# Kernel tuning notes

Measured on AMD Instinct MI355X. Metric: run time of the kernel, lower is better.

The kernel has to match this reference:

```python
import jax, jax.numpy as jnp
import numpy as np
import math

B, S, D, N, H = 4, 2048, 1024, 512, 8
HD = D // H  # head_dim = 128
LN_EPS = 1e-5


def setup_inputs() -> dict:
    key = jax.random.key(0)
    ks = jax.random.split(key, 12)
    return {
        "query": jax.random.normal(ks[0], (B, S, D), jnp.float32),
        "memory_weights": jax.random.uniform(ks[1], (B, S, N), jnp.float32),
        "update_input": jax.random.normal(ks[2], (B, S, D), jnp.float32),
        "memory_keys": jax.random.normal(ks[3], (N, D), jnp.float32),
        "memory_values": jax.random.normal(ks[4], (N, D), jnp.float32),
        "memory_decay": jnp.float32(0.95),
        "gate_w": jax.random.normal(ks[5], (2 * D, D), jnp.float32) / math.sqrt(2 * D),
        "gate_b": jnp.zeros((D,), jnp.float32),
        "out_w": jax.random.normal(ks[6], (D, D), jnp.float32) / math.sqrt(D),
        "out_b": jnp.zeros((D,), jnp.float32),
        "ln_gamma": jnp.ones((D,), jnp.float32),
        "ln_beta": jnp.zeros((D,), jnp.float32),
    }


def reference(query, memory_weights, update_input, memory_keys, memory_values,
              memory_decay, gate_w, gate_b, out_w, out_b, ln_gamma, ln_beta):
    # Multi-head attention read: einsum 'bshd,nhd->bsn' sums over h and d,
    # so it equals a full [D]-dot product; only the scale uses head_dim.
    scores = jnp.einsum("bsd,nd->bsn", query, memory_keys) / math.sqrt(HD)
    scores = scores * memory_weights  # multiplicative mask before softmax
    probs = jax.nn.softmax(scores, axis=-1)
    memory_read = jnp.einsum("bsn,nd->bsd", probs, memory_values)
    memory_read = memory_read * memory_decay

    # Gated update path (update_input provided)
    gate_in = jnp.concatenate([memory_read, update_input], axis=-1)  # [B,S,2D]
    gate = jax.nn.sigmoid(gate_in @ gate_w + gate_b)  # [B,S,D]
    # NOTE: the no_grad EMA update of memory_values is a side effect that does
    # not influence this forward output; omitted from the pure reference.
    memory_read = memory_read * (1.0 + jnp.mean(gate, axis=-1, keepdims=True))

    out = memory_read @ out_w + out_b  # output projection (dropout = eval identity)
    mu = jnp.mean(out, axis=-1, keepdims=True)
    var = jnp.var(out, axis=-1, keepdims=True)
    out = (out - mu) * jax.lax.rsqrt(var + LN_EPS) * ln_gamma + ln_beta
    return out
```

## Files before the change

### kernel.cpp

```cpp
#include <hip/hip_runtime.h>
#include <hip/hip_bf16.h>

typedef __attribute__((ext_vector_type(8))) short bf16x8;
typedef __attribute__((ext_vector_type(4))) float f32x4;
typedef __attribute__((ext_vector_type(4))) int i32x4;
typedef __attribute__((ext_vector_type(2))) int i32x2;
typedef __attribute__((ext_vector_type(4))) unsigned short u16x4;

static __device__ __forceinline__ void gload_lds16(const void* g, void* l) {
  __builtin_amdgcn_global_load_lds((const __attribute__((address_space(1))) void*)g,
                                   (__attribute__((address_space(3))) void*)l,
                                   16, 0, 0);
}

static __device__ __forceinline__ unsigned short f2bf(float x) {
  unsigned int u = __float_as_uint(x);
  u += 0x7fffu + ((u >> 16) & 1u);
  return (unsigned short)(u >> 16);
}
static __device__ __forceinline__ float bf2f(unsigned short u) {
  return __uint_as_float((unsigned int)u << 16);
}

__global__ __launch_bounds__(256)
void prep(const float* __restrict__ ob, int* __restrict__ flag,
          float* __restrict__ zeros,
          const float* __restrict__ mk, const float* __restrict__ mv,
          unsigned short* __restrict__ kb, unsigned short* __restrict__ mvb,
          const float* __restrict__ ow, unsigned short* __restrict__ owt,
          const float* __restrict__ q, unsigned short* __restrict__ qb)
{
  __shared__ float t[32][33];
  const int b = blockIdx.x;
  const int tid = threadIdx.x;
  if (b == 0) {
    f32x4 v = *(const f32x4*)(ob + tid * 4);
    float mx = fmaxf(fmaxf(fabsf(v[0]), fabsf(v[1])), fmaxf(fabsf(v[2]), fabsf(v[3])));
#pragma unroll
    for (int off = 32; off >= 1; off >>= 1) mx = fmaxf(mx, __shfl_xor(mx, off, 64));
    __shared__ float sm[4];
    const int wid = tid >> 6, lane = tid & 63;
    if (lane == 0) sm[wid] = mx;
    __syncthreads();
    if (tid == 0) {
      float m = fmaxf(fmaxf(sm[0], sm[1]), fmaxf(sm[2], sm[3]));
      *flag = (m != 0.0f) ? 1 : 0;
    }
  } else if (b < 17) {
    f32x4 z = {};
    *(f32x4*)(zeros + (b - 1) * 1024 + tid * 4) = z;
  } else if (b < 529) {
    int idx = (b - 17) * 256 + tid;
    const float* in; unsigned short* out; int rel;
    if (idx < 65536) { in = mk; out = kb;  rel = idx; }
    else             { in = mv; out = mvb; rel = idx - 65536; }
    size_t f = (size_t)rel * 8;
    f32x4 a = *(const f32x4*)(in + f);
    f32x4 c = *(const f32x4*)(in + f + 4);
    union { unsigned short u[8]; i32x4 vec; } pk;
#pragma unroll
    for (int i = 0; i < 4; ++i) { pk.u[i] = f2bf(a[i]); pk.u[4 + i] = f2bf(c[i]); }
    *(i32x4*)(out + f) = pk.vec;
  } else if (b < 1553) {
    int id = b - 529;
    const int bx = id & 31, by = id >> 5;
    const int tx = tid & 31, ty = tid >> 5;
    const int c0 = bx * 32, r0 = by * 32;
#pragma unroll
    for (int i = 0; i < 4; ++i)
      t[ty + i * 8][tx] = ow[(size_t)(r0 + ty + i * 8) * 1024 + c0 + tx];
    __syncthreads();
#pragma unroll
    for (int i = 0; i < 4; ++i)
      owt[(size_t)(c0 + ty + i * 8) * 1024 + r0 + tx] = f2bf(t[tx][ty + i * 8]);
  } else {
    int idx = (b - 1553) * 256 + tid;
    size_t f = (size_t)idx * 8;
    f32x4 a = *(const f32x4*)(q + f);
    f32x4 c = *(const f32x4*)(q + f + 4);
    union { unsigned short u[8]; i32x4 vec; } pk;
#pragma unroll
    for (int i = 0; i < 4; ++i) { pk.u[i] = f2bf(a[i]); pk.u[4 + i] = f2bf(c[i]); }
    *(i32x4*)(qb + f) = pk.vec;
  }
}

__global__ __launch_bounds__(256)
void prep_gated(const float* __restrict__ upd, unsigned short* __restrict__ cat,
                const float* __restrict__ gw, unsigned short* __restrict__ gwt,
                const float* __restrict__ mv, unsigned short* __restrict__ vt,
                const int* __restrict__ flag)
{
  if (*flag == 0) return;
  __shared__ float t[32][33];
  const int b = blockIdx.x;
  const int tid = threadIdx.x;
  if (b < 4096) {
    int idx = b * 256 + tid;
    size_t f = (size_t)idx * 8;
    int row = (int)(f >> 10);
    int col = (int)(f & 1023);
    f32x4 a = *(const f32x4*)(upd + f);
    f32x4 c = *(const f32x4*)(upd + f + 4);
    union { unsigned short u[8]; i32x4 vec; } pk;
#pragma unroll
    for (int i = 0; i < 4; ++i) { pk.u[i] = f2bf(a[i]); pk.u[4 + i] = f2bf(c[i]); }
    *(i32x4*)(cat + (size_t)row * 2048 + 1024 + col) = pk.vec;
  } else {
    const float* in; unsigned short* out; int R, id;
    if (b < 6144) { in = gw; out = gwt; R = 2048; id = b - 4096; }
    else          { in = mv; out = vt;  R = 512;  id = b - 6144; }
    const int bx = id & 31, by = id >> 5;
    const int tx = tid & 31, ty = tid >> 5;
    const int c0 = bx * 32, r0 = by * 32;
#pragma unroll
    for (int i = 0; i < 4; ++i)
      t[ty + i * 8][tx] = in[(size_t)(r0 + ty + i * 8) * 1024 + c0 + tx];
    __syncthreads();
#pragma unroll
    for (int i = 0; i < 4; ++i)
      out[(size_t)(c0 + ty + i * 8) * R + r0 + tx] = f2bf(t[tx][ty + i * 8]);
  }
}

template <int EPI, int BN>
__global__ __launch_bounds__(256)
void gemm_bt(const unsigned short* __restrict__ A, int lda,
             const unsigned short* __restrict__ Bt, int ldb,
             int Kd, int Nd,
             unsigned short* __restrict__ Cb, int ldcb,
             const float* __restrict__ bias,
             float* __restrict__ rowsum,
             const float* __restrict__ fscale,
             const int* __restrict__ flag)
{
  if (flag != nullptr && *flag == 0) return;
  constexpr int NB = BN / 32;
  __shared__ unsigned short As[128 * 64];
  __shared__ unsigned short Bs[BN * 64];
  const int tid  = threadIdx.x;
  const int wid  = tid >> 6;
  const int lane = tid & 63;

  const int nwg  = gridDim.x * gridDim.y;
  const int flat = blockIdx.y * gridDim.x + blockIdx.x;
  const int swz  = (flat & 7) * (nwg >> 3) + (flat >> 3);
  const int bx   = swz % gridDim.x;
  const int by   = swz / gridDim.x;

  const int brow = by * 128;
  const int bcol = bx * BN;
  const int wr = wid >> 1, wc = wid & 1;
  const int l15 = lane & 15, l4 = lane >> 4;

  f32x4 acc[4][NB] = {};
  const int foff = wid * 512 + lane * 8;

  for (int k0 = 0; k0 < Kd; k0 += 64) {
#pragma unroll
    for (int c = 0; c < 4; ++c) {
      int f = c * 2048 + foff;
      int r = f >> 6, kc = f & 63;
      gload_lds16(A + (size_t)(brow + r) * lda + k0 + kc, As + c * 2048 + wid * 512);
    }
#pragma unroll
    for (int c = 0; c < NB; ++c) {
      int f = c * 2048 + foff;
      int r = f >> 6, kc = f & 63;
      gload_lds16(Bt + (size_t)(bcol + r) * ldb + k0 + kc, Bs + c * 2048 + wid * 512);
    }
    __syncthreads();
#pragma unroll
    for (int kk = 0; kk < 2; ++kk) {
      const int ko = kk * 32 + l4 * 8;
      bf16x8 af[4], bfv[NB];
#pragma unroll
      for (int m = 0; m < 4; ++m)
        af[m] = *(const bf16x8*)(As + (wr * 64 + m * 16 + l15) * 64 + ko);
#pragma unroll
      for (int n = 0; n < NB; ++n)
        bfv[n] = *(const bf16x8*)(Bs + (wc * (BN / 2) + n * 16 + l15) * 64 + ko);
#pragma unroll
      for (int m = 0; m < 4; ++m)
#pragma unroll
        for (int n = 0; n < NB; ++n)
          acc[m][n] = __builtin_amdgcn_mfma_f32_16x16x32_bf16(af[m], bfv[n], acc[m][n], 0, 0, 0);
    }
    __syncthreads();
  }

  if constexpr (EPI == 2) {
#pragma unroll
    for (int m = 0; m < 4; ++m) {
#pragma unroll
      for (int j = 0; j < 4; ++j) {
        float part = 0.0f;
#pragma unroll
        for (int n = 0; n < NB; ++n) {
          int col = bcol + wc * (BN / 2) + n * 16 + l15;
          float x = acc[m][n][j] + bias[col];
          part += 1.0f / (1.0f + __expf(-x));
        }
#pragma unroll
        for (int off = 1; off < 16; off <<= 1)
          part += __shfl_xor(part, off, 64);
        if (l15 == 0) {
          int row = brow + wr * 64 + m * 16 + l4 * 4 + j;
          atomicAdd(&rowsum[row], part);
        }
      }
    }
  } else if constexpr (EPI == 5) {
#pragma unroll
    for (int m = 0; m < 4; ++m) {
#pragma unroll
      for (int j = 0; j < 4; ++j) {
        int row = brow + wr * 64 + m * 16 + l4 * 4 + j;
        const float* mwrow = bias + (size_t)row * Nd;
        float part = 0.0f;
#pragma unroll
        for (int n = 0; n < NB; ++n) {
          int col = bcol + wc * (BN / 2) + n * 16 + l15;
          float p = __expf(acc[m][n][j] * 0.08838834764831845f * mwrow[col]);
          part += p;
          Cb[(size_t)row * ldcb + col] = f2bf(p);
        }
#pragma unroll
        for (int off = 1; off < 16; off <<= 1)
          part += __shfl_xor(part, off, 64);
        if (l15 == 0) atomicAdd(&rowsum[row], part);
      }
    }
  } else {
    float fs = 1.0f;
    if constexpr (EPI == 1) fs = *fscale;
#pragma unroll
    for (int m = 0; m < 4; ++m) {
      int row0 = brow + wr * 64 + m * 16 + l4 * 4;
#pragma unroll
      for (int j = 0; j < 4; ++j) {
        int row = row0 + j;
        const float rscl = fs / rowsum[row];
#pragma unroll
        for (int n = 0; n < NB; ++n) {
          int col = bcol + wc * (BN / 2) + n * 16 + l15;
          Cb[(size_t)row * ldcb + col] = f2bf(acc[m][n][j] * rscl);
        }
      }
    }
  }
}

__global__ __launch_bounds__(256)
void w2_partial(const unsigned short* __restrict__ owt,
                const unsigned short* __restrict__ mvb,
                float* __restrict__ w2p)
{
  __shared__ unsigned short As[128 * 64];
  __shared__ unsigned short Bs[128 * 64];
  const int tid  = threadIdx.x;
  const int wid  = tid >> 6;
  const int lane = tid & 63;
  const int brow = blockIdx.y * 128;
  const int bcol = blockIdx.x * 128;
  const int kbeg = blockIdx.z * 128;
  const int wr = wid >> 1, wc = wid & 1;
  const int l15 = lane & 15, l4 = lane >> 4;

  f32x4 acc[4][4] = {};
  const int foff = wid * 512 + lane * 8;

  for (int k0 = kbeg; k0 < kbeg + 128; k0 += 64) {
#pragma unroll
    for (int c = 0; c < 4; ++c) {
      int f = c * 2048 + foff;
      int r = f >> 6, kc = f & 63;
      gload_lds16(owt + (size_t)(brow + r) * 1024 + k0 + kc, As + c * 2048 + wid * 512);
    }
#pragma unroll
    for (int c = 0; c < 4; ++c) {
      int f = c * 2048 + foff;
      int r = f >> 6, kc = f & 63;
      gload_lds16(mvb + (size_t)(bcol + r) * 1024 + k0 + kc, Bs + c * 2048 + wid * 512);
    }
    __syncthreads();
#pragma unroll
    for (int kk = 0; kk < 2; ++kk) {
      const int ko = kk * 32 + l4 * 8;
      bf16x8 af[4], bfv[4];
#pragma unroll
      for (int m = 0; m < 4; ++m)
        af[m] = *(const bf16x8*)(As + (wr * 64 + m * 16 + l15) * 64 + ko);
#pragma unroll
      for (int n = 0; n < 4; ++n)
        bfv[n] = *(const bf16x8*)(Bs + (wc * 64 + n * 16 + l15) * 64 + ko);
#pragma unroll
      for (int m = 0; m < 4; ++m)
#pragma unroll
        for (int n = 0; n < 4; ++n)
          acc[m][n] = __builtin_amdgcn_mfma_f32_16x16x32_bf16(af[m], bfv[n], acc[m][n], 0, 0, 0);
    }
    __syncthreads();
  }

  float* dst = w2p + (size_t)blockIdx.z * 524288;
#pragma unroll
  for (int m = 0; m < 4; ++m) {
    int row0 = brow + wr * 64 + m * 16 + l4 * 4;
#pragma unroll
    for (int j = 0; j < 4; ++j) {
      int row = row0 + j;
#pragma unroll
      for (int n = 0; n < 4; ++n) {
        int col = bcol + wc * 64 + n * 16 + l15;
        dst[(size_t)row * 512 + col] = acc[m][n][j];
      }
    }
  }
}

__global__ __launch_bounds__(256)
void w2_reduce(const float* __restrict__ w2p, unsigned short* __restrict__ w2t,
               const float* __restrict__ dec)
{
  const int i = (blockIdx.x * 256 + threadIdx.x) * 4;
  const float d = *dec;
  f32x4 s = {};
#pragma unroll
  for (int sl = 0; sl < 8; ++sl) {
    f32x4 p = *(const f32x4*)(w2p + (size_t)sl * 524288 + i);
    s[0] += p[0]; s[1] += p[1]; s[2] += p[2]; s[3] += p[3];
  }
  union { unsigned short u[4]; i32x2 v; } pk;
#pragma unroll
  for (int j = 0; j < 4; ++j) pk.u[j] = f2bf(s[j] * d);
  *(i32x2*)(w2t + i) = pk.v;
}

__global__ __launch_bounds__(256)
void ln_rows(const unsigned short* __restrict__ X, const float* __restrict__ gsum,
             const float* __restrict__ ob,
             const float* __restrict__ gamma, const float* __restrict__ beta,
             float* __restrict__ Y)
{
  const int row = blockIdx.x;
  const int tid = threadIdx.x;
  const size_t base = (size_t)row * 1024 + tid * 4;
  const float scl = 1.0f + gsum[row] * (1.0f / 1024.0f);
  u16x4 xr = *(const u16x4*)(X + base);
  f32x4 bo = *(const f32x4*)(ob + tid * 4);
  float x[4];
#pragma unroll
  for (int i = 0; i < 4; ++i) x[i] = bf2f(xr[i]) * scl + bo[i];
  float s = x[0] + x[1] + x[2] + x[3];
  float q = x[0] * x[0] + x[1] * x[1] + x[2] * x[2] + x[3] * x[3];
#pragma unroll
  for (int off = 32; off >= 1; off >>= 1) {
    s += __shfl_xor(s, off, 64);
    q += __shfl_xor(q, off, 64);
  }
  __shared__ float ss[4], qq[4];
  const int wid = tid >> 6, lane = tid & 63;
  if (lane == 0) { ss[wid] = s; qq[wid] = q; }
  __syncthreads();
  s = ss[0] + ss[1] + ss[2] + ss[3];
  q = qq[0] + qq[1] + qq[2] + qq[3];
  const float mu = s * (1.0f / 1024.0f);
  const float var = q * (1.0f / 1024.0f) - mu * mu;
  const float r = rsqrtf(var + 1e-5f);
  f32x4 g = *(const f32x4*)(gamma + tid * 4);
  f32x4 b = *(const f32x4*)(beta + tid * 4);
  f32x4 y;
#pragma unroll
  for (int i = 0; i < 4; ++i) y[i] = (x[i] - mu) * r * g[i] + b[i];
  *(f32x4*)(Y + base) = y;
}

extern "C" void kernel_launch(void* const* d_in, const int* in_sizes, int n_in,
                              void* d_out, int out_size, void* d_ws, size_t ws_size,
                              hipStream_t stream)
{
  (void)in_sizes; (void)n_in; (void)out_size; (void)ws_size;
  const float* q   = (const float*)d_in[0];
  const float* mw  = (const float*)d_in[1];
  const float* upd = (const float*)d_in[2];
  const float* mk  = (const float*)d_in[3];
  const float* mv  = (const float*)d_in[4];
  const float* dec = (const float*)d_in[5];
  const float* gw  = (const float*)d_in[6];
  const float* gb  = (const float*)d_in[7];
  const float* ow  = (const float*)d_in[8];
  const float* ob  = (const float*)d_in[9];
  const float* lg  = (const float*)d_in[10];
  const float* lb  = (const float*)d_in[11];
  float* outp = (float*)d_out;
  char* ws = (char*)d_ws;

  unsigned short* qb     = (unsigned short*)(ws + 0);
  unsigned short* probs  = (unsigned short*)(ws + 16777216);
  unsigned short* outpre = (unsigned short*)(ws + 25165824);
  unsigned short* kb     = (unsigned short*)(ws + 41943040);
  unsigned short* mvb    = (unsigned short*)(ws + 42991616);
  unsigned short* owt    = (unsigned short*)(ws + 44040192);
  unsigned short* w2t    = (unsigned short*)(ws + 46137344);
  float*          w2p    = (float*)(ws + 47185920);
  unsigned short* vt     = (unsigned short*)(ws + 63963136);
  unsigned short* gwt    = (unsigned short*)(ws + 65011712);
  unsigned short* cat    = (unsigned short*)(ws + 69206016);
  float*          gsum   = (float*)(ws + 102760448);
  float*          rowsum = (float*)(ws + 102793216);
  int*            flag   = (int*)(ws + 102825984);

  prep<<<5649, 256, 0, stream>>>(ob, flag, gsum, mk, mv, kb, mvb, ow, owt, q, qb);
  prep_gated<<<6656, 256, 0, stream>>>(upd, cat, gw, gwt, mv, vt, flag);

  gemm_bt<5, 64><<<dim3(8, 64), 256, 0, stream>>>(qb, 1024, kb, 1024, 1024, 512,
                                                  probs, 512, mw, rowsum, nullptr, nullptr);
  w2_partial<<<dim3(4, 8, 8), 256, 0, stream>>>(owt, mvb, w2p);
  w2_reduce<<<512, 256, 0, stream>>>(w2p, w2t, dec);
  gemm_bt<1, 128><<<dim3(8, 64), 256, 0, stream>>>(probs, 512, vt, 512, 512, 1024,
                                                   cat, 2048, nullptr, rowsum, dec, flag);
  gemm_bt<2, 128><<<dim3(8, 64), 256, 0, stream>>>(cat, 2048, gwt, 2048, 2048, 1024,
                                                   nullptr, 0, gb, gsum, nullptr, flag);
  gemm_bt<6, 128><<<dim3(8, 64), 256, 0, stream>>>(probs, 512, w2t, 512, 512, 1024,
                                                   outpre, 1024, nullptr, rowsum, nullptr, nullptr);
  ln_rows<<<8192, 256, 0, stream>>>(outpre, gsum, ob, lg, lb, outp);
}
```

Measured before the change: 88.08 us.

## Merge independent GEMM stages into shared launches to cut kernel count

Independent stages are packed into shared grids. The two prep kernels become one launch, where the gated-path blocks recompute the out_b nonzero check locally. The scores GEMM shares a launch with a 4-way split-K W2 partial GEMM, the W2 reduction shares one with the memory-read GEMM, and the output projection shares one with the gate GEMM. This cuts launches from nine to five and lets independent work fill the machine together, at the cost of fewer split-K slices and heterogeneous blocks within a grid.

```diff
diff --git a/kernel.cpp b/kernel.cpp
--- a/kernel.cpp
+++ b/kernel.cpp
@@ -20,6 +20,55 @@
 }
 static __device__ __forceinline__ float bf2f(unsigned short u) {
   return __uint_as_float((unsigned int)u << 16);
+}
+
+template <int BN>
+static __device__ __forceinline__ void gemm_core(
+    const unsigned short* __restrict__ A, int lda,
+    const unsigned short* __restrict__ Bt, int ldb,
+    int kbeg, int kend, int brow, int bcol,
+    unsigned short* As, unsigned short* Bs,
+    f32x4 (&acc)[4][BN / 32])
+{
+  constexpr int NB = BN / 32;
+  const int tid = threadIdx.x;
+  const int wid = tid >> 6, lane = tid & 63;
+  const int wr = wid >> 1, wc = wid & 1;
+  const int l15 = lane & 15, l4 = lane >> 4;
+  const int foff = wid * 512 + lane * 8;
+
+  for (int k0 = kbeg; k0 < kend; k0 += 64) {
+#pragma unroll
+    for (int c = 0; c < 4; ++c) {
+      int f = c * 2048 + foff;
+      gload_lds16(A + (size_t)(brow + (f >> 6)) * lda + k0 + (f & 63),
+                  As + c * 2048 + wid * 512);
+    }
+#pragma unroll
+    for (int c = 0; c < NB; ++c) {
+      int f = c * 2048 + foff;
+      gload_lds16(Bt + (size_t)(bcol + (f >> 6)) * ldb + k0 + (f & 63),
+                  Bs + c * 2048 + wid * 512);
+    }
+    __syncthreads();
+#pragma unroll
+    for (int kk = 0; kk < 2; ++kk) {
+      const int ko = kk * 32 + l4 * 8;
+      bf16x8 af[4], bfv[NB];
+#pragma unroll
+      for (int m = 0; m < 4; ++m)
+        af[m] = *(const bf16x8*)(As + (wr * 64 + m * 16 + l15) * 64 + ko);
+#pragma unroll
+      for (int n = 0; n < NB; ++n)
+        bfv[n] = *(const bf16x8*)(Bs + (wc * (BN / 2) + n * 16 + l15) * 64 + ko);
+#pragma unroll
+      for (int m = 0; m < 4; ++m)
+#pragma unroll
+        for (int n = 0; n < NB; ++n)
+          acc[m][n] = __builtin_amdgcn_mfma_f32_16x16x32_bf16(af[m], bfv[n], acc[m][n], 0, 0, 0);
+    }
+    __syncthreads();
+  }
 }
 
 __global__ __launch_bounds__(256)
@@ -28,7 +77,10 @@
           const float* __restrict__ mk, const float* __restrict__ mv,
           unsigned short* __restrict__ kb, unsigned short* __restrict__ mvb,
           const float* __restrict__ ow, unsigned short* __restrict__ owt,
-          const float* __restrict__ q, unsigned short* __restrict__ qb)
+          const float* __restrict__ q, unsigned short* __restrict__ qb,
+          const float* __restrict__ upd, unsigned short* __restrict__ cat,
+          const float* __restrict__ gw, unsigned short* __restrict__ gwt,
+          unsigned short* __restrict__ vt)
 {
   __shared__ float t[32][33];
   const int b = blockIdx.x;
@@ -73,7 +125,7 @@
 #pragma unroll
     for (int i = 0; i < 4; ++i)
       owt[(size_t)(c0 + ty + i * 8) * 1024 + r0 + tx] = f2bf(t[tx][ty + i * 8]);
-  } else {
+  } else if (b < 5649) {
     int idx = (b - 1553) * 256 + tid;
     size_t f = (size_t)idx * 8;
     f32x4 a = *(const f32x4*)(q + f);
@@ -82,123 +134,224 @@
 #pragma unroll
     for (int i = 0; i < 4; ++i) { pk.u[i] = f2bf(a[i]); pk.u[4 + i] = f2bf(c[i]); }
     *(i32x4*)(qb + f) = pk.vec;
+  } else {
+    f32x4 v = *(const f32x4*)(ob + tid * 4);
+    float mx = fmaxf(fmaxf(fabsf(v[0]), fabsf(v[1])), fmaxf(fabsf(v[2]), fabsf(v[3])));
+#pragma unroll
+    for (int off = 32; off >= 1; off >>= 1) mx = fmaxf(mx, __shfl_xor(mx, off, 64));
+    __shared__ float sm2[4];
+    const int wid = tid >> 6, lane = tid & 63;
+    if (lane == 0) sm2[wid] = mx;
+    __syncthreads();
+    float m = fmaxf(fmaxf(sm2[0], sm2[1]), fmaxf(sm2[2], sm2[3]));
+    if (m == 0.0f) return;
+    __syncthreads();
+    int g = b - 5649;
+    if (g < 4096) {
+      int idx = g * 256 + tid;
+      size_t f = (size_t)idx * 8;
+      int row = (int)(f >> 10);
+      int col = (int)(f & 1023);
+      f32x4 a = *(const f32x4*)(upd + f);
+      f32x4 c = *(const f32x4*)(upd + f + 4);
+      union { unsigned short u[8]; i32x4 vec; } pk;
+#pragma unroll
+      for (int i = 0; i < 4; ++i) { pk.u[i] = f2bf(a[i]); pk.u[4 + i] = f2bf(c[i]); }
+      *(i32x4*)(cat + (size_t)row * 2048 + 1024 + col) = pk.vec;
+    } else {
+      const float* in; unsigned short* out; int R, id;
+      if (g < 6144) { in = gw; out = gwt; R = 2048; id = g - 4096; }
+      else          { in = mv; out = vt;  R = 512;  id = g - 6144; }
+      const int bx = id & 31, by = id >> 5;
+      const int tx = tid & 31, ty = tid >> 5;
+      const int c0 = bx * 32, r0 = by * 32;
+#pragma unroll
+      for (int i = 0; i < 4; ++i)
+        t[ty + i * 8][tx] = in[(size_t)(r0 + ty + i * 8) * 1024 + c0 + tx];
+      __syncthreads();
+#pragma unroll
+      for (int i = 0; i < 4; ++i)
+        out[(size_t)(c0 + ty + i * 8) * R + r0 + tx] = f2bf(t[tx][ty + i * 8]);
+    }
   }
 }
 
 __global__ __launch_bounds__(256)
-void prep_gated(const float* __restrict__ upd, unsigned short* __restrict__ cat,
-                const float* __restrict__ gw, unsigned short* __restrict__ gwt,
-                const float* __restrict__ mv, unsigned short* __restrict__ vt,
-                const int* __restrict__ flag)
-{
-  if (*flag == 0) return;
-  __shared__ float t[32][33];
+void k_scores_w2(const unsigned short* __restrict__ qb,
+                 const unsigned short* __restrict__ kb,
+                 const float* __restrict__ mw,
+                 unsigned short* __restrict__ probs,
+                 float* __restrict__ rowsum,
+                 const unsigned short* __restrict__ owt,
+                 const unsigned short* __restrict__ mvb,
+                 float* __restrict__ w2p)
+{
+  __shared__ unsigned short As[128 * 64];
+  __shared__ unsigned short Bs[128 * 64];
   const int b = blockIdx.x;
   const int tid = threadIdx.x;
-  if (b < 4096) {
-    int idx = b * 256 + tid;
-    size_t f = (size_t)idx * 8;
-    int row = (int)(f >> 10);
-    int col = (int)(f & 1023);
-    f32x4 a = *(const f32x4*)(upd + f);
-    f32x4 c = *(const f32x4*)(upd + f + 4);
-    union { unsigned short u[8]; i32x4 vec; } pk;
-#pragma unroll
-    for (int i = 0; i < 4; ++i) { pk.u[i] = f2bf(a[i]); pk.u[4 + i] = f2bf(c[i]); }
-    *(i32x4*)(cat + (size_t)row * 2048 + 1024 + col) = pk.vec;
-  } else {
-    const float* in; unsigned short* out; int R, id;
-    if (b < 6144) { in = gw; out = gwt; R = 2048; id = b - 4096; }
-    else          { in = mv; out = vt;  R = 512;  id = b - 6144; }
-    const int bx = id & 31, by = id >> 5;
-    const int tx = tid & 31, ty = tid >> 5;
-    const int c0 = bx * 32, r0 = by * 32;
-#pragma unroll
-    for (int i = 0; i < 4; ++i)
-      t[ty + i * 8][tx] = in[(size_t)(r0 + ty + i * 8) * 1024 + c0 + tx];
-    __syncthreads();
-#pragma unroll
-    for (int i = 0; i < 4; ++i)
-      out[(size_t)(c0 + ty + i * 8) * R + r0 + tx] = f2bf(t[tx][ty + i * 8]);
-  }
-}
-
-template <int EPI, int BN>
-__global__ __launch_bounds__(256)
-void gemm_bt(const unsigned short* __restrict__ A, int lda,
-             const unsigned short* __restrict__ Bt, int ldb,
-             int Kd, int Nd,
-             unsigned short* __restrict__ Cb, int ldcb,
-             const float* __restrict__ bias,
-             float* __restrict__ rowsum,
-             const float* __restrict__ fscale,
-             const int* __restrict__ flag)
-{
-  if (flag != nullptr && *flag == 0) return;
-  constexpr int NB = BN / 32;
-  __shared__ unsigned short As[128 * 64];
-  __shared__ unsigned short Bs[BN * 64];
-  const int tid  = threadIdx.x;
-  const int wid  = tid >> 6;
-  const int lane = tid & 63;
-
-  const int nwg  = gridDim.x * gridDim.y;
-  const int flat = blockIdx.y * gridDim.x + blockIdx.x;
-  const int swz  = (flat & 7) * (nwg >> 3) + (flat >> 3);
-  const int bx   = swz % gridDim.x;
-  const int by   = swz / gridDim.x;
-
-  const int brow = by * 128;
-  const int bcol = bx * BN;
+  const int wid = tid >> 6, lane = tid & 63;
   const int wr = wid >> 1, wc = wid & 1;
   const int l15 = lane & 15, l4 = lane >> 4;
 
-  f32x4 acc[4][NB] = {};
-  const int foff = wid * 512 + lane * 8;
-
-  for (int k0 = 0; k0 < Kd; k0 += 64) {
-#pragma unroll
-    for (int c = 0; c < 4; ++c) {
-      int f = c * 2048 + foff;
-      int r = f >> 6, kc = f & 63;
-      gload_lds16(A + (size_t)(brow + r) * lda + k0 + kc, As + c * 2048 + wid * 512);
-    }
-#pragma unroll
-    for (int c = 0; c < NB; ++c) {
-      int f = c * 2048 + foff;
-      int r = f >> 6, kc = f & 63;
-      gload_lds16(Bt + (size_t)(bcol + r) * ldb + k0 + kc, Bs + c * 2048 + wid * 512);
-    }
-    __syncthreads();
-#pragma unroll
-    for (int kk = 0; kk < 2; ++kk) {
-      const int ko = kk * 32 + l4 * 8;
-      bf16x8 af[4], bfv[NB];
-#pragma unroll
-      for (int m = 0; m < 4; ++m)
-        af[m] = *(const bf16x8*)(As + (wr * 64 + m * 16 + l15) * 64 + ko);
-#pragma unroll
-      for (int n = 0; n < NB; ++n)
-        bfv[n] = *(const bf16x8*)(Bs + (wc * (BN / 2) + n * 16 + l15) * 64 + ko);
-#pragma unroll
-      for (int m = 0; m < 4; ++m)
-#pragma unroll
-        for (int n = 0; n < NB; ++n)
-          acc[m][n] = __builtin_amdgcn_mfma_f32_16x16x32_bf16(af[m], bfv[n], acc[m][n], 0, 0, 0);
-    }
-    __syncthreads();
-  }
-
-  if constexpr (EPI == 2) {
+  if (b < 128) {
+    const int brow = ((b >> 2) & 7) * 128;
+    const int bcol = (b & 3) * 128;
+    const int kbeg = (b >> 5) * 256;
+    f32x4 acc[4][4] = {};
+    gemm_core<128>(owt, 1024, mvb, 1024, kbeg, kbeg + 256, brow, bcol, As, Bs, acc);
+    float* dst = w2p + (size_t)(b >> 5) * 524288;
+#pragma unroll
+    for (int m = 0; m < 4; ++m) {
+      int row0 = brow + wr * 64 + m * 16 + l4 * 4;
+#pragma unroll
+      for (int j = 0; j < 4; ++j) {
+#pragma unroll
+        for (int n = 0; n < 4; ++n)
+          dst[(size_t)(row0 + j) * 512 + bcol + wc * 64 + n * 16 + l15] = acc[m][n][j];
+      }
+    }
+  } else {
+    const int f = b - 128;
+    const int swz = (f & 7) * 64 + (f >> 3);
+    const int bx = swz & 7, by = swz >> 3;
+    const int brow = by * 128, bcol = bx * 64;
+    f32x4 acc[4][2] = {};
+    gemm_core<64>(qb, 1024, kb, 1024, 0, 1024, brow, bcol, As, Bs, acc);
+#pragma unroll
+    for (int m = 0; m < 4; ++m) {
+#pragma unroll
+      for (int j = 0; j < 4; ++j) {
+        int row = brow + wr * 64 + m * 16 + l4 * 4 + j;
+        const float* mwrow = mw + (size_t)row * 512;
+        float part = 0.0f;
+#pragma unroll
+        for (int n = 0; n < 2; ++n) {
+          int col = bcol + wc * 32 + n * 16 + l15;
+          float p = __expf(acc[m][n][j] * 0.08838834764831845f * mwrow[col]);
+          part += p;
+          probs[(size_t)row * 512 + col] = f2bf(p);
+        }
+#pragma unroll
+        for (int off = 1; off < 16; off <<= 1)
+          part += __shfl_xor(part, off, 64);
+        if (l15 == 0) atomicAdd(&rowsum[row], part);
+      }
+    }
+  }
+}
+
+__global__ __launch_bounds__(256)
+void k_w2red_read(const float* __restrict__ w2p, unsigned short* __restrict__ w2t,
+                  const float* __restrict__ dec,
+                  const unsigned short* __restrict__ probs,
+                  const unsigned short* __restrict__ vt,
+                  unsigned short* __restrict__ cat,
+                  const float* __restrict__ rowsum,
+                  const int* __restrict__ flag)
+{
+  __shared__ unsigned short As[128 * 64];
+  __shared__ unsigned short Bs[128 * 64];
+  const int b = blockIdx.x;
+  const int tid = threadIdx.x;
+  if (b < 512) {
+    const int i = (b * 256 + tid) * 4;
+    const float d = *dec;
+    f32x4 s = {};
+#pragma unroll
+    for (int sl = 0; sl < 4; ++sl) {
+      f32x4 p = *(const f32x4*)(w2p + (size_t)sl * 524288 + i);
+      s[0] += p[0]; s[1] += p[1]; s[2] += p[2]; s[3] += p[3];
+    }
+    union { unsigned short u[4]; i32x2 v; } pk;
+#pragma unroll
+    for (int j = 0; j < 4; ++j) pk.u[j] = f2bf(s[j] * d);
+    *(i32x2*)(w2t + i) = pk.v;
+  } else {
+    if (*flag == 0) return;
+    const int f = b - 512;
+    const int swz = (f & 7) * 64 + (f >> 3);
+    const int bx = swz & 7, by = swz >> 3;
+    const int brow = by * 128, bcol = bx * 128;
+    const int wid = tid >> 6, lane = tid & 63;
+    const int wr = wid >> 1, wc = wid & 1;
+    const int l15 = lane & 15, l4 = lane >> 4;
+    f32x4 acc[4][4] = {};
+    gemm_core<128>(probs, 512, vt, 512, 0, 512, brow, bcol, As, Bs, acc);
+    const float d = *dec;
+#pragma unroll
+    for (int m = 0; m < 4; ++m) {
+      int row0 = brow + wr * 64 + m * 16 + l4 * 4;
+#pragma unroll
+      for (int j = 0; j < 4; ++j) {
+        int row = row0 + j;
+        const float rscl = d / rowsum[row];
+#pragma unroll
+        for (int n = 0; n < 4; ++n) {
+          int col = bcol + wc * 64 + n * 16 + l15;
+          cat[(size_t)row * 2048 + col] = f2bf(acc[m][n][j] * rscl);
+        }
+      }
+    }
+  }
+}
+
+__global__ __launch_bounds__(256)
+void k_out_gate(const unsigned short* __restrict__ probs,
+                const unsigned short* __restrict__ w2t,
+                const float* __restrict__ rowsum,
+                unsigned short* __restrict__ outpre,
+                const unsigned short* __restrict__ cat,
+                const unsigned short* __restrict__ gwt,
+                const float* __restrict__ gb,
+                float* __restrict__ gsum,
+                const int* __restrict__ flag)
+{
+  __shared__ unsigned short As[128 * 64];
+  __shared__ unsigned short Bs[128 * 64];
+  const int b = blockIdx.x;
+  const int tid = threadIdx.x;
+  const int wid = tid >> 6, lane = tid & 63;
+  const int wr = wid >> 1, wc = wid & 1;
+  const int l15 = lane & 15, l4 = lane >> 4;
+
+  if (b < 512) {
+    const int swz = (b & 7) * 64 + (b >> 3);
+    const int bx = swz & 7, by = swz >> 3;
+    const int brow = by * 128, bcol = bx * 128;
+    f32x4 acc[4][4] = {};
+    gemm_core<128>(probs, 512, w2t, 512, 0, 512, brow, bcol, As, Bs, acc);
+#pragma unroll
+    for (int m = 0; m < 4; ++m) {
+      int row0 = brow + wr * 64 + m * 16 + l4 * 4;
+#pragma unroll
+      for (int j = 0; j < 4; ++j) {
+        int row = row0 + j;
+        const float rscl = 1.0f / rowsum[row];
+#pragma unroll
+        for (int n = 0; n < 4; ++n) {
+          int col = bcol + wc * 64 + n * 16 + l15;
+          outpre[(size_t)row * 1024 + col] = f2bf(acc[m][n][j] * rscl);
+        }
+      }
+    }
+  } else {
+    if (*flag == 0) return;
+    const int f = b - 512;
+    const int swz = (f & 7) * 64 + (f >> 3);
+    const int bx = swz & 7, by = swz >> 3;
+    const int brow = by * 128, bcol = bx * 128;
+    f32x4 acc[4][4] = {};
+    gemm_core<128>(cat, 2048, gwt, 2048, 0, 2048, brow, bcol, As, Bs, acc);
 #pragma unroll
     for (int m = 0; m < 4; ++m) {
 #pragma unroll
       for (int j = 0; j < 4; ++j) {
         float part = 0.0f;
 #pragma unroll
-        for (int n = 0; n < NB; ++n) {
-          int col = bcol + wc * (BN / 2) + n * 16 + l15;
-          float x = acc[m][n][j] + bias[col];
+        for (int n = 0; n < 4; ++n) {
+          int col = bcol + wc * 64 + n * 16 + l15;
+          float x = acc[m][n][j] + gb[col];
           part += 1.0f / (1.0f + __expf(-x));
         }
 #pragma unroll
@@ -206,135 +359,11 @@
           part += __shfl_xor(part, off, 64);
         if (l15 == 0) {
           int row = brow + wr * 64 + m * 16 + l4 * 4 + j;
-          atomicAdd(&rowsum[row], part);
+          atomicAdd(&gsum[row], part);
         }
       }
     }
-  } else if constexpr (EPI == 5) {
-#pragma unroll
-    for (int m = 0; m < 4; ++m) {
-#pragma unroll
-      for (int j = 0; j < 4; ++j) {
-        int row = brow + wr * 64 + m * 16 + l4 * 4 + j;
-        const float* mwrow = bias + (size_t)row * Nd;
-        float part = 0.0f;
-#pragma unroll
-        for (int n = 0; n < NB; ++n) {
-          int col = bcol + wc * (BN / 2) + n * 16 + l15;
-          float p = __expf(acc[m][n][j] * 0.08838834764831845f * mwrow[col]);
-          part += p;
-          Cb[(size_t)row * ldcb + col] = f2bf(p);
-        }
-#pragma unroll
-        for (int off = 1; off < 16; off <<= 1)
-          part += __shfl_xor(part, off, 64);
-        if (l15 == 0) atomicAdd(&rowsum[row], part);
-      }
-    }
-  } else {
-    float fs = 1.0f;
-    if constexpr (EPI == 1) fs = *fscale;
-#pragma unroll
-    for (int m = 0; m < 4; ++m) {
-      int row0 = brow + wr * 64 + m * 16 + l4 * 4;
-#pragma unroll
-      for (int j = 0; j < 4; ++j) {
-        int row = row0 + j;
-        const float rscl = fs / rowsum[row];
-#pragma unroll
-        for (int n = 0; n < NB; ++n) {
-          int col = bcol + wc * (BN / 2) + n * 16 + l15;
-          Cb[(size_t)row * ldcb + col] = f2bf(acc[m][n][j] * rscl);
-        }
-      }
-    }
-  }
-}
-
-__global__ __launch_bounds__(256)
-void w2_partial(const unsigned short* __restrict__ owt,
-                const unsigned short* __restrict__ mvb,
-                float* __restrict__ w2p)
-{
-  __shared__ unsigned short As[128 * 64];
-  __shared__ unsigned short Bs[128 * 64];
-  const int tid  = threadIdx.x;
-  const int wid  = tid >> 6;
-  const int lane = tid & 63;
-  const int brow = blockIdx.y * 128;
-  const int bcol = blockIdx.x * 128;
-  const int kbeg = blockIdx.z * 128;
-  const int wr = wid >> 1, wc = wid & 1;
-  const int l15 = lane & 15, l4 = lane >> 4;
-
-  f32x4 acc[4][4] = {};
-  const int foff = wid * 512 + lane * 8;
-
-  for (int k0 = kbeg; k0 < kbeg + 128; k0 += 64) {
-#pragma unroll
-    for (int c = 0; c < 4; ++c) {
-      int f = c * 2048 + foff;
-      int r = f >> 6, kc = f & 63;
-      gload_lds16(owt + (size_t)(brow + r) * 1024 + k0 + kc, As + c * 2048 + wid * 512);
-    }
-#pragma unroll
-    for (int c = 0; c < 4; ++c) {
-      int f = c * 2048 + foff;
-      int r = f >> 6, kc = f & 63;
-      gload_lds16(mvb + (size_t)(bcol + r) * 1024 + k0 + kc, Bs + c * 2048 + wid * 512);
-    }
-    __syncthreads();
-#pragma unroll
-    for (int kk = 0; kk < 2; ++kk) {
-      const int ko = kk * 32 + l4 * 8;
-      bf16x8 af[4], bfv[4];
-#pragma unroll
-      for (int m = 0; m < 4; ++m)
-        af[m] = *(const bf16x8*)(As + (wr * 64 + m * 16 + l15) * 64 + ko);
-#pragma unroll
-      for (int n = 0; n < 4; ++n)
-        bfv[n] = *(const bf16x8*)(Bs + (wc * 64 + n * 16 + l15) * 64 + ko);
-#pragma unroll
-      for (int m = 0; m < 4; ++m)
-#pragma unroll
-        for (int n = 0; n < 4; ++n)
-          acc[m][n] = __builtin_amdgcn_mfma_f32_16x16x32_bf16(af[m], bfv[n], acc[m][n], 0, 0, 0);
-    }
-    __syncthreads();
-  }
-
-  float* dst = w2p + (size_t)blockIdx.z * 524288;
-#pragma unroll
-  for (int m = 0; m < 4; ++m) {
-    int row0 = brow + wr * 64 + m * 16 + l4 * 4;
-#pragma unroll
-    for (int j = 0; j < 4; ++j) {
-      int row = row0 + j;
-#pragma unroll
-      for (int n = 0; n < 4; ++n) {
-        int col = bcol + wc * 64 + n * 16 + l15;
-        dst[(size_t)row * 512 + col] = acc[m][n][j];
-      }
-    }
-  }
-}
-
-__global__ __launch_bounds__(256)
-void w2_reduce(const float* __restrict__ w2p, unsigned short* __restrict__ w2t,
-               const float* __restrict__ dec)
-{
-  const int i = (blockIdx.x * 256 + threadIdx.x) * 4;
-  const float d = *dec;
-  f32x4 s = {};
-#pragma unroll
-  for (int sl = 0; sl < 8; ++sl) {
-    f32x4 p = *(const f32x4*)(w2p + (size_t)sl * 524288 + i);
-    s[0] += p[0]; s[1] += p[1]; s[2] += p[2]; s[3] += p[3];
-  }
-  union { unsigned short u[4]; i32x2 v; } pk;
-#pragma unroll
-  for (int j = 0; j < 4; ++j) pk.u[j] = f2bf(s[j] * d);
-  *(i32x2*)(w2t + i) = pk.v;
+  }
 }
 
 __global__ __launch_bounds__(256)
@@ -369,10 +398,10 @@
   const float var = q * (1.0f / 1024.0f) - mu * mu;
   const float r = rsqrtf(var + 1e-5f);
   f32x4 g = *(const f32x4*)(gamma + tid * 4);
-  f32x4 b = *(const f32x4*)(beta + tid * 4);
+  f32x4 bt = *(const f32x4*)(beta + tid * 4);
   f32x4 y;
 #pragma unroll
-  for (int i = 0; i < 4; ++i) y[i] = (x[i] - mu) * r * g[i] + b[i];
+  for (int i = 0; i < 4; ++i) y[i] = (x[i] - mu) * r * g[i] + bt[i];
   *(f32x4*)(Y + base) = y;
 }
 
@@ -404,25 +433,17 @@
   unsigned short* owt    = (unsigned short*)(ws + 44040192);
   unsigned short* w2t    = (unsigned short*)(ws + 46137344);
   float*          w2p    = (float*)(ws + 47185920);
-  unsigned short* vt     = (unsigned short*)(ws + 63963136);
-  unsigned short* gwt    = (unsigned short*)(ws + 65011712);
-  unsigned short* cat    = (unsigned short*)(ws + 69206016);
-  float*          gsum   = (float*)(ws + 102760448);
-  float*          rowsum = (float*)(ws + 102793216);
-  int*            flag   = (int*)(ws + 102825984);
-
-  prep<<<5649, 256, 0, stream>>>(ob, flag, gsum, mk, mv, kb, mvb, ow, owt, q, qb);
-  prep_gated<<<6656, 256, 0, stream>>>(upd, cat, gw, gwt, mv, vt, flag);
-
-  gemm_bt<5, 64><<<dim3(8, 64), 256, 0, stream>>>(qb, 1024, kb, 1024, 1024, 512,
-                                                  probs, 512, mw, rowsum, nullptr, nullptr);
-  w2_partial<<<dim3(4, 8, 8), 256, 0, stream>>>(owt, mvb, w2p);
-  w2_reduce<<<512, 256, 0, stream>>>(w2p, w2t, dec);
-  gemm_bt<1, 128><<<dim3(8, 64), 256, 0, stream>>>(probs, 512, vt, 512, 512, 1024,
-                                                   cat, 2048, nullptr, rowsum, dec, flag);
-  gemm_bt<2, 128><<<dim3(8, 64), 256, 0, stream>>>(cat, 2048, gwt, 2048, 2048, 1024,
-                                                   nullptr, 0, gb, gsum, nullptr, flag);
-  gemm_bt<6, 128><<<dim3(8, 64), 256, 0, stream>>>(probs, 512, w2t, 512, 512, 1024,
-                                                   outpre, 1024, nullptr, rowsum, nullptr, nullptr);
+  unsigned short* vt     = (unsigned short*)(ws + 55574528);
+  unsigned short* gwt    = (unsigned short*)(ws + 56623104);
+  unsigned short* cat    = (unsigned short*)(ws + 60817408);
+  float*          gsum   = (float*)(ws + 94371840);
+  float*          rowsum = (float*)(ws + 94404608);
+  int*            flag   = (int*)(ws + 94437376);
+
+  prep<<<12305, 256, 0, stream>>>(ob, flag, gsum, mk, mv, kb, mvb, ow, owt,
+                                  q, qb, upd, cat, gw, gwt, vt);
+  k_scores_w2<<<640, 256, 0, stream>>>(qb, kb, mw, probs, rowsum, owt, mvb, w2p);
+  k_w2red_read<<<1024, 256, 0, stream>>>(w2p, w2t, dec, probs, vt, cat, rowsum, flag);
+  k_out_gate<<<1024, 256, 0, stream>>>(probs, w2t, rowsum, outpre, cat, gwt, gb, gsum, flag);
   ln_rows<<<8192, 256, 0, stream>>>(outpre, gsum, ob, lg, lb, outp);
 }
```

Result: faster. 81.75 us (-7.2%).
